# Performance work log

Hardware: AMD Instinct MI355X
Metric: run time of the kernel (lower is better)

## Reference

```python
import jax, jax.numpy as jnp
import numpy as np

B, T, D, H = 4, 4096, 1024, 64

def setup_inputs() -> dict:
    key = jax.random.key(0)
    k1, k2, k3, k4 = jax.random.split(key, 4)
    x = jax.random.normal(k1, (B, T, D), dtype=jnp.float32)
    Wk = jax.random.normal(k2, (D, H), dtype=jnp.float32) * (D ** -0.5)
    Wq = jax.random.normal(k3, (D, H), dtype=jnp.float32) * (D ** -0.5)
    Wv = jax.random.normal(k4, (D, H), dtype=jnp.float32) * (D ** -0.5)
    return {"x": x, "Wk": Wk, "Wq": Wq, "Wv": Wv}

def reference(x, Wk, Wq, Wv):
    # single-head causal self-attention (dropout inactive: training=False)
    k = x @ Wk  # [B,T,H]
    q = x @ Wq  # [B,T,H]
    v = x @ Wv  # [B,T,H]
    scale = jnp.float32(1.0) / jnp.sqrt(jnp.float32(H))
    wei = jnp.einsum('bth,bsh->bts', q, k) * scale  # [B,T,T]
    t = x.shape[1]
    causal = jnp.tril(jnp.ones((t, t), dtype=bool))[None, :, :]
    wei = jnp.where(causal, wei, jnp.float32(-jnp.inf))
    wei = jax.nn.softmax(wei, axis=-1)
    out = jnp.einsum('bts,bsh->bth', wei, v)  # [B,T,H]
    return out
```

## Files before the change

### kernel.cpp

```cpp
#include <hip/hip_runtime.h>

typedef __bf16 bf16_t;
typedef __bf16 bf16x8 __attribute__((ext_vector_type(8)));
typedef __bf16 bf16x4 __attribute__((ext_vector_type(4)));
typedef float  f32x4  __attribute__((ext_vector_type(4)));
typedef float  f32x16 __attribute__((ext_vector_type(16)));

#define B_  4
#define T_  4096
#define H_  64
#define BT  (B_*T_)

#define QSCALE 0.1803368801111204f

#define NSLOT_PB 576
#define NSLOT    2304

#define WS_KFR  0x000000u
#define WS_QFR  0x200000u
#define WS_VFR  0x400000u
#define WS_WT   0x600000u
#define WS_POUT 0x680000u
#define WS_PL   0xF80000u

#define MFMA16(a,b,c) __builtin_amdgcn_mfma_f32_16x16x32_bf16((a),(b),(c),0,0,0)
#define MFMA32(a,b,c) __builtin_amdgcn_mfma_f32_32x32x16_bf16((a),(b),(c),0,0,0)

__device__ __forceinline__ unsigned pk2(float a, float b) {
  union { __bf16 h[2]; unsigned u; } u_;
  u_.h[0] = (__bf16)a; u_.h[1] = (__bf16)b;
  return u_.u;
}

__device__ __forceinline__ f32x16 zero16() {
  f32x16 z;
#pragma unroll
  for (int i = 0; i < 16; ++i) z[i] = 0.f;
  return z;
}

__global__ __launch_bounds__(256) void wtrans_kernel(
    const float* __restrict__ Wk, const float* __restrict__ Wq,
    const float* __restrict__ Wv, bf16_t* __restrict__ WT) {
  __shared__ float lw[64][65];
  int w  = blockIdx.x >> 4;
  int kc = blockIdx.x & 15;
  const float* W = (w == 0) ? Wk : (w == 1) ? Wq : Wv;
  float sc = (w == 1) ? QSCALE : 1.0f;
  int t = threadIdx.x;
  int rr = t >> 2, c0 = (t & 3) * 16;
  const float* src = W + (size_t)(kc*64 + rr)*64 + c0;
#pragma unroll
  for (int j = 0; j < 4; ++j) {
    float4 v = *reinterpret_cast<const float4*>(src + j*4);
    lw[rr][c0+j*4+0] = v.x; lw[rr][c0+j*4+1] = v.y;
    lw[rr][c0+j*4+2] = v.z; lw[rr][c0+j*4+3] = v.w;
  }
  __syncthreads();
  int nl = t >> 2, kl0 = (t & 3) * 16;
  bf16_t* dst = WT + (size_t)(w*64 + nl)*1024 + kc*64 + kl0;
  bf16x8 o0, o1;
#pragma unroll
  for (int j = 0; j < 8; ++j) o0[j] = (bf16_t)(lw[kl0+j][nl] * sc);
#pragma unroll
  for (int j = 0; j < 8; ++j) o1[j] = (bf16_t)(lw[kl0+8+j][nl] * sc);
  *reinterpret_cast<bf16x8*>(dst)     = o0;
  *reinterpret_cast<bf16x8*>(dst + 8) = o1;
}

__global__ __launch_bounds__(256) void proj_kernel(
    const float* __restrict__ x, const bf16_t* __restrict__ WT,
    bf16_t* __restrict__ kfr, bf16_t* __restrict__ qfr, bf16_t* __restrict__ vfr) {
  __shared__ __bf16 xs[2][32][72];
  int tid  = threadIdx.x;
  int wv   = tid >> 6;
  int lane = tid & 63;
  int col  = lane & 15;
  int g    = lane >> 4;
  int m0   = blockIdx.x * 32;
  int nbase = wv * 48;

  f32x4 zero4 = {0.f, 0.f, 0.f, 0.f};
  f32x4 acc[2][3];
#pragma unroll
  for (int i = 0; i < 2; ++i)
#pragma unroll
    for (int j = 0; j < 3; ++j) acc[i][j] = zero4;

  int srow = tid >> 3;
  int scol = (tid & 7) * 8;
  const float* xrow = x + (size_t)(m0 + srow)*1024 + scol;

  float4 a0 = *reinterpret_cast<const float4*>(xrow);
  float4 a1 = *reinterpret_cast<const float4*>(xrow + 4);
  float4 b0 = *reinterpret_cast<const float4*>(xrow + 64);
  float4 b1 = *reinterpret_cast<const float4*>(xrow + 68);
  {
    bf16x8 pk = { (bf16_t)a0.x,(bf16_t)a0.y,(bf16_t)a0.z,(bf16_t)a0.w,
                  (bf16_t)a1.x,(bf16_t)a1.y,(bf16_t)a1.z,(bf16_t)a1.w };
    *reinterpret_cast<bf16x8*>(&xs[0][srow][scol]) = pk;
  }

  for (int t = 0; t < 16; ++t) {
    int kc = t * 64;
    int cur = t & 1;
    __syncthreads();
    if (t + 2 < 16) {
      const float* p = xrow + (t+2)*64;
      if ((t & 1) == 0) { a0 = *reinterpret_cast<const float4*>(p);
                          a1 = *reinterpret_cast<const float4*>(p + 4); }
      else              { b0 = *reinterpret_cast<const float4*>(p);
                          b1 = *reinterpret_cast<const float4*>(p + 4); }
    }
#pragma unroll
    for (int kk = 0; kk < 2; ++kk) {
      int ko = kk*32 + g*8;
      bf16x8 f0 = *(const bf16x8*)&xs[cur][ 0 + col][ko];
      bf16x8 f1 = *(const bf16x8*)&xs[cur][16 + col][ko];
#pragma unroll
      for (int nti = 0; nti < 3; ++nti) {
        const bf16_t* wp = WT + (size_t)(nbase + nti*16 + col)*1024 + kc + ko;
        bf16x8 bfr = *(const bf16x8*)wp;
        acc[0][nti] = MFMA16(f0, bfr, acc[0][nti]);
        acc[1][nti] = MFMA16(f1, bfr, acc[1][nti]);
      }
    }
    if (t + 1 < 16) {
      bf16x8 pk;
      if ((t & 1) == 0)
        pk = bf16x8{ (bf16_t)b0.x,(bf16_t)b0.y,(bf16_t)b0.z,(bf16_t)b0.w,
                     (bf16_t)b1.x,(bf16_t)b1.y,(bf16_t)b1.z,(bf16_t)b1.w };
      else
        pk = bf16x8{ (bf16_t)a0.x,(bf16_t)a0.y,(bf16_t)a0.z,(bf16_t)a0.w,
                     (bf16_t)a1.x,(bf16_t)a1.y,(bf16_t)a1.z,(bf16_t)a1.w };
      *reinterpret_cast<bf16x8*>(&xs[cur^1][srow][scol]) = pk;
    }
  }
#pragma unroll
  for (int mt = 0; mt < 2; ++mt) {
    int row0 = m0 + mt*16 + 4*g;
#pragma unroll
    for (int nti = 0; nti < 3; ++nti) {
      int n = nbase + nti*16 + col;
      f32x4 v = acc[mt][nti];
      if (n < 128) {
        int h = n & 63;
        bf16_t* base = (n < 64) ? kfr : qfr;
#pragma unroll
        for (int r = 0; r < 4; ++r) {
          int t2 = row0 + r;
          size_t idx = (size_t)((t2>>6)*8 + ((t2>>5)&1)*4 + (h>>4))*512
                     + (size_t)((t2&31) + ((h>>3)&1)*32)*8 + (h&7);
          base[idx] = (bf16_t)v[r];
        }
      } else {
        int h = n - 128;
        size_t idx = (size_t)((row0>>6)*8 + ((h>>5)&1)*4 + ((row0>>4)&3))*512
                   + (size_t)((h&31) + ((row0>>3)&1)*32)*8 + (row0&7);
        bf16x4 pk = { (bf16_t)v[0], (bf16_t)v[1], (bf16_t)v[2], (bf16_t)v[3] };
        *reinterpret_cast<bf16x4*>(&vfr[idx]) = pk;
      }
    }
  }
}

__global__ __launch_bounds__(64) void attn_kernel(
    const bf16_t* __restrict__ qfr, const bf16_t* __restrict__ kfr,
    const bf16_t* __restrict__ vfr, bf16_t* __restrict__ pout,
    float* __restrict__ pl) {
  int l  = threadIdx.x;
  int ql = l & 31;
  int hi = l >> 5;

  int bidx = blockIdx.x;
  int b = bidx / NSLOT_PB;
  int s = bidx - b * NSLOT_PB;
  s = NSLOT_PB - 1 - s;
  int a = 0;
#pragma unroll
  for (int aa = 1; aa < 8; ++aa) if (8*aa*(aa+1) <= s) a = aa;
  int r2 = s - 8*a*(a+1);
  int qd = r2 / (a+1);
  int c  = r2 - qd*(a+1);
  int jt = 16*a + qd;
  int slot = b*NSLOT_PB + s;

  int q0    = jt << 5;
  int kv_lo = c << 9;
  int kv_hi = min(kv_lo + 512, q0 + 32);
  int ntiles = (kv_hi - kv_lo + 63) >> 6;
  int qg = q0 + ql;

  const bf16_t* qb = qfr + (size_t)((b*T_ + q0) >> 6)*4096
                   + (size_t)((q0 >> 5) & 1)*2048 + l*8;
  bf16x8 qf0 = *(const bf16x8*)(qb);
  bf16x8 qf1 = *(const bf16x8*)(qb + 512);
  bf16x8 qf2 = *(const bf16x8*)(qb + 1024);
  bf16x8 qf3 = *(const bf16x8*)(qb + 1536);

  const bf16_t* kfb = kfr + (size_t)(b*T_)*64 + l*8;
  const bf16_t* vfb = vfr + (size_t)(b*T_)*64 + l*8;

  bf16x8 kA0,kA1,kA2,kA3, kB0,kB1,kB2,kB3;
#define LOADK(kvt_) do { const bf16_t* kp_ = kfb + (size_t)(kvt_)*64;          \
    kA0=*(const bf16x8*)(kp_);        kA1=*(const bf16x8*)(kp_+512);           \
    kA2=*(const bf16x8*)(kp_+1024);   kA3=*(const bf16x8*)(kp_+1536);          \
    kB0=*(const bf16x8*)(kp_+2048);   kB1=*(const bf16x8*)(kp_+2560);          \
    kB2=*(const bf16x8*)(kp_+3072);   kB3=*(const bf16x8*)(kp_+3584); } while(0)

  LOADK(kv_lo);

  f32x16 oA = zero16(), oB = zero16();
  float l_ = 0.f;

  for (int t = 0; t < ntiles; ++t) {
    int kvt = kv_lo + t*64;
    const bf16_t* vp = vfb + (size_t)kvt*64;
    bf16x8 vA0 = *(const bf16x8*)(vp);
    bf16x8 vA1 = *(const bf16x8*)(vp + 512);
    bf16x8 vA2 = *(const bf16x8*)(vp + 1024);
    bf16x8 vA3 = *(const bf16x8*)(vp + 1536);
    bf16x8 vB0 = *(const bf16x8*)(vp + 2048);
    bf16x8 vB1 = *(const bf16x8*)(vp + 2560);
    bf16x8 vB2 = *(const bf16x8*)(vp + 3072);
    bf16x8 vB3 = *(const bf16x8*)(vp + 3584);

    f32x16 sA = zero16(), sB = zero16();
    sA = MFMA32(kA0, qf0, sA); sB = MFMA32(kB0, qf0, sB);
    sA = MFMA32(kA1, qf1, sA); sB = MFMA32(kB1, qf1, sB);
    sA = MFMA32(kA2, qf2, sA); sB = MFMA32(kB2, qf2, sB);
    sA = MFMA32(kA3, qf3, sA); sB = MFMA32(kB3, qf3, sB);

    if (t + 1 < ntiles) LOADK(kvt + 64);

    if (kvt + 63 > q0) {
#pragma unroll
      for (int r = 0; r < 16; ++r) {
        int kvo = kvt + (r&3) + 8*(r>>2) + 4*hi;
        if (kvo > qg)      sA[r] = -1e30f;
        if (kvo + 32 > qg) sB[r] = -1e30f;
      }
    }

    float pA[16], pB[16];
    float ts = 0.f;
#pragma unroll
    for (int r = 0; r < 16; ++r) { pA[r] = exp2f(sA[r]); ts += pA[r]; }
#pragma unroll
    for (int r = 0; r < 16; ++r) { pB[r] = exp2f(sB[r]); ts += pB[r]; }
    l_ += ts + __shfl_xor(ts, 32);

    bf16x8 p0, p1, p2, p3;
#define MKSLICES(P, F0, F1) do {                                               \
    unsigned w0 = pk2(P[0],P[1]),   w1 = pk2(P[2],P[3]);                       \
    unsigned w2 = pk2(P[4],P[5]),   w3 = pk2(P[6],P[7]);                       \
    unsigned w4 = pk2(P[8],P[9]),   w5 = pk2(P[10],P[11]);                     \
    unsigned w6 = pk2(P[12],P[13]), w7 = pk2(P[14],P[15]);                     \
    unsigned x0 = (unsigned)__shfl_xor((int)w0,32);                            \
    unsigned x1 = (unsigned)__shfl_xor((int)w1,32);                            \
    unsigned x2 = (unsigned)__shfl_xor((int)w2,32);                            \
    unsigned x3 = (unsigned)__shfl_xor((int)w3,32);                            \
    unsigned x4 = (unsigned)__shfl_xor((int)w4,32);                            \
    unsigned x5 = (unsigned)__shfl_xor((int)w5,32);                            \
    unsigned x6 = (unsigned)__shfl_xor((int)w6,32);                            \
    unsigned x7 = (unsigned)__shfl_xor((int)w7,32);                            \
    union { unsigned d[4]; bf16x8 v; } u0_, u1_;                               \
    u0_.d[0] = hi ? x2 : w0;  u0_.d[1] = hi ? x3 : w1;                         \
    u0_.d[2] = hi ? w2 : x0;  u0_.d[3] = hi ? w3 : x1;                         \
    u1_.d[0] = hi ? x6 : w4;  u1_.d[1] = hi ? x7 : w5;                         \
    u1_.d[2] = hi ? w6 : x4;  u1_.d[3] = hi ? w7 : x5;                         \
    F0 = u0_.v; F1 = u1_.v; } while(0)
    MKSLICES(pA, p0, p1);
    MKSLICES(pB, p2, p3);

    oA = MFMA32(vA0, p0, oA); oB = MFMA32(vB0, p0, oB);
    oA = MFMA32(vA1, p1, oA); oB = MFMA32(vB1, p1, oB);
    oA = MFMA32(vA2, p2, oA); oB = MFMA32(vB2, p2, oB);
    oA = MFMA32(vA3, p3, oA); oB = MFMA32(vB3, p3, oB);
  }

  bf16_t* po = pout + (size_t)slot * 2048;
#pragma unroll
  for (int r = 0; r < 16; ++r) {
    int h = (r&3) + 8*(r>>2) + 4*hi;
    po[h*32 + ql]      = (bf16_t)oA[r];
    po[(h+32)*32 + ql] = (bf16_t)oB[r];
  }
  if (l < 32) pl[(size_t)slot*32 + l] = l_;
}

__global__ __launch_bounds__(256) void combine_kernel(
    const bf16_t* __restrict__ pout, const float* __restrict__ pl,
    float* __restrict__ out) {
  int blk = blockIdx.x;
  int b  = blk >> 7;
  int jt = blk & 127;
  int tid = threadIdx.x;
  int wv = tid >> 6;
  int l  = tid & 63;
  int a  = jt >> 4;
  int nch = a + 1;
  int slot0 = b*NSLOT_PB + 8*a*(a+1) + (jt & 15)*(a+1);

  float oacc[8], lacc[8];
#pragma unroll
  for (int q = 0; q < 8; ++q) { oacc[q] = 0.f; lacc[q] = 0.f; }
  for (int c2 = 0; c2 < nch; ++c2) {
    const bf16_t* pp = pout + (size_t)(slot0 + c2)*2048 + l*32 + wv*8;
    bf16x8 o8 = *(const bf16x8*)pp;
    const float* plc = pl + (size_t)(slot0 + c2)*32 + wv*8;
#pragma unroll
    for (int q = 0; q < 8; ++q) { oacc[q] += (float)o8[q]; lacc[q] += plc[q]; }
  }
  float* op = out + ((size_t)b*T_ + (size_t)jt*32 + wv*8)*64 + l;
#pragma unroll
  for (int q = 0; q < 8; ++q) op[(size_t)q*64] = oacc[q] / lacc[q];
}

extern "C" void kernel_launch(void* const* d_in, const int* in_sizes, int n_in,
                              void* d_out, int out_size, void* d_ws, size_t ws_size,
                              hipStream_t stream) {
  (void)in_sizes; (void)n_in; (void)out_size; (void)ws_size;
  const float* x  = (const float*)d_in[0];
  const float* Wk = (const float*)d_in[1];
  const float* Wq = (const float*)d_in[2];
  const float* Wv = (const float*)d_in[3];
  char* ws = (char*)d_ws;
  bf16_t* kfr  = (bf16_t*)(ws + WS_KFR);
  bf16_t* qfr  = (bf16_t*)(ws + WS_QFR);
  bf16_t* vfr  = (bf16_t*)(ws + WS_VFR);
  bf16_t* WT   = (bf16_t*)(ws + WS_WT);
  bf16_t* pout = (bf16_t*)(ws + WS_POUT);
  float*  pl   = (float*)(ws + WS_PL);
  float*  outp = (float*)d_out;

  hipLaunchKernelGGL(wtrans_kernel,  dim3(48),    dim3(256), 0, stream, Wk, Wq, Wv, WT);
  hipLaunchKernelGGL(proj_kernel,    dim3(512),   dim3(256), 0, stream, x, WT, kfr, qfr, vfr);
  hipLaunchKernelGGL(attn_kernel,    dim3(NSLOT), dim3(64),  0, stream, qfr, kfr, vfr, pout, pl);
  hipLaunchKernelGGL(combine_kernel, dim3(512),   dim3(256), 0, stream, pout, pl, outp);
}
```

Before: 70.71 us.

## Halve KV split chunk, widen projection blocks, and raise MFMA wave priority

```diff
diff --git a/kernel.cpp b/kernel.cpp
--- a/kernel.cpp
+++ b/kernel.cpp
@@ -13,15 +13,15 @@
 
 #define QSCALE 0.1803368801111204f
 
-#define NSLOT_PB 576
-#define NSLOT    2304
-
-#define WS_KFR  0x000000u
-#define WS_QFR  0x200000u
-#define WS_VFR  0x400000u
-#define WS_WT   0x600000u
-#define WS_POUT 0x680000u
-#define WS_PL   0xF80000u
+#define NSLOT_PB 1088
+#define NSLOT    4352
+
+#define WS_KFR  0x0000000u
+#define WS_QFR  0x0200000u
+#define WS_VFR  0x0400000u
+#define WS_WT   0x0600000u
+#define WS_POUT 0x0680000u
+#define WS_PL   0x1780000u
 
 #define MFMA16(a,b,c) __builtin_amdgcn_mfma_f32_16x16x32_bf16((a),(b),(c),0,0,0)
 #define MFMA32(a,b,c) __builtin_amdgcn_mfma_f32_32x32x16_bf16((a),(b),(c),0,0,0)
@@ -68,98 +68,81 @@
   *reinterpret_cast<bf16x8*>(dst + 8) = o1;
 }
 
-__global__ __launch_bounds__(256) void proj_kernel(
+__global__ __launch_bounds__(512) void proj_kernel(
     const float* __restrict__ x, const bf16_t* __restrict__ WT,
     bf16_t* __restrict__ kfr, bf16_t* __restrict__ qfr, bf16_t* __restrict__ vfr) {
   __shared__ __bf16 xs[2][32][72];
   int tid  = threadIdx.x;
   int wv   = tid >> 6;
+  int wm   = wv >> 2;
+  int wn   = wv & 3;
   int lane = tid & 63;
   int col  = lane & 15;
   int g    = lane >> 4;
   int m0   = blockIdx.x * 32;
-  int nbase = wv * 48;
+  int nbase = wn * 48;
 
   f32x4 zero4 = {0.f, 0.f, 0.f, 0.f};
-  f32x4 acc[2][3];
-#pragma unroll
-  for (int i = 0; i < 2; ++i)
-#pragma unroll
-    for (int j = 0; j < 3; ++j) acc[i][j] = zero4;
-
-  int srow = tid >> 3;
-  int scol = (tid & 7) * 8;
+  f32x4 acc[3] = {zero4, zero4, zero4};
+
+  int srow = tid >> 4;
+  int scol = (tid & 15) * 4;
   const float* xrow = x + (size_t)(m0 + srow)*1024 + scol;
 
   float4 a0 = *reinterpret_cast<const float4*>(xrow);
-  float4 a1 = *reinterpret_cast<const float4*>(xrow + 4);
   float4 b0 = *reinterpret_cast<const float4*>(xrow + 64);
-  float4 b1 = *reinterpret_cast<const float4*>(xrow + 68);
   {
-    bf16x8 pk = { (bf16_t)a0.x,(bf16_t)a0.y,(bf16_t)a0.z,(bf16_t)a0.w,
-                  (bf16_t)a1.x,(bf16_t)a1.y,(bf16_t)a1.z,(bf16_t)a1.w };
-    *reinterpret_cast<bf16x8*>(&xs[0][srow][scol]) = pk;
+    bf16x4 pk = { (bf16_t)a0.x,(bf16_t)a0.y,(bf16_t)a0.z,(bf16_t)a0.w };
+    *reinterpret_cast<bf16x4*>(&xs[0][srow][scol]) = pk;
   }
 
   for (int t = 0; t < 16; ++t) {
+    __syncthreads();
     int kc = t * 64;
     int cur = t & 1;
-    __syncthreads();
     if (t + 2 < 16) {
       const float* p = xrow + (t+2)*64;
-      if ((t & 1) == 0) { a0 = *reinterpret_cast<const float4*>(p);
-                          a1 = *reinterpret_cast<const float4*>(p + 4); }
-      else              { b0 = *reinterpret_cast<const float4*>(p);
-                          b1 = *reinterpret_cast<const float4*>(p + 4); }
+      if ((t & 1) == 0) a0 = *reinterpret_cast<const float4*>(p);
+      else              b0 = *reinterpret_cast<const float4*>(p);
     }
 #pragma unroll
     for (int kk = 0; kk < 2; ++kk) {
       int ko = kk*32 + g*8;
-      bf16x8 f0 = *(const bf16x8*)&xs[cur][ 0 + col][ko];
-      bf16x8 f1 = *(const bf16x8*)&xs[cur][16 + col][ko];
+      bf16x8 f0 = *(const bf16x8*)&xs[cur][wm*16 + col][ko];
 #pragma unroll
       for (int nti = 0; nti < 3; ++nti) {
         const bf16_t* wp = WT + (size_t)(nbase + nti*16 + col)*1024 + kc + ko;
         bf16x8 bfr = *(const bf16x8*)wp;
-        acc[0][nti] = MFMA16(f0, bfr, acc[0][nti]);
-        acc[1][nti] = MFMA16(f1, bfr, acc[1][nti]);
+        acc[nti] = MFMA16(f0, bfr, acc[nti]);
       }
     }
     if (t + 1 < 16) {
-      bf16x8 pk;
-      if ((t & 1) == 0)
-        pk = bf16x8{ (bf16_t)b0.x,(bf16_t)b0.y,(bf16_t)b0.z,(bf16_t)b0.w,
-                     (bf16_t)b1.x,(bf16_t)b1.y,(bf16_t)b1.z,(bf16_t)b1.w };
-      else
-        pk = bf16x8{ (bf16_t)a0.x,(bf16_t)a0.y,(bf16_t)a0.z,(bf16_t)a0.w,
-                     (bf16_t)a1.x,(bf16_t)a1.y,(bf16_t)a1.z,(bf16_t)a1.w };
-      *reinterpret_cast<bf16x8*>(&xs[cur^1][srow][scol]) = pk;
-    }
-  }
-#pragma unroll
-  for (int mt = 0; mt < 2; ++mt) {
-    int row0 = m0 + mt*16 + 4*g;
-#pragma unroll
-    for (int nti = 0; nti < 3; ++nti) {
-      int n = nbase + nti*16 + col;
-      f32x4 v = acc[mt][nti];
-      if (n < 128) {
-        int h = n & 63;
-        bf16_t* base = (n < 64) ? kfr : qfr;
-#pragma unroll
-        for (int r = 0; r < 4; ++r) {
-          int t2 = row0 + r;
-          size_t idx = (size_t)((t2>>6)*8 + ((t2>>5)&1)*4 + (h>>4))*512
-                     + (size_t)((t2&31) + ((h>>3)&1)*32)*8 + (h&7);
-          base[idx] = (bf16_t)v[r];
-        }
-      } else {
-        int h = n - 128;
-        size_t idx = (size_t)((row0>>6)*8 + ((h>>5)&1)*4 + ((row0>>4)&3))*512
-                   + (size_t)((h&31) + ((row0>>3)&1)*32)*8 + (row0&7);
-        bf16x4 pk = { (bf16_t)v[0], (bf16_t)v[1], (bf16_t)v[2], (bf16_t)v[3] };
-        *reinterpret_cast<bf16x4*>(&vfr[idx]) = pk;
+      float4 sv = ((t & 1) == 0) ? b0 : a0;
+      bf16x4 pk = { (bf16_t)sv.x,(bf16_t)sv.y,(bf16_t)sv.z,(bf16_t)sv.w };
+      *reinterpret_cast<bf16x4*>(&xs[cur^1][srow][scol]) = pk;
+    }
+  }
+  int row0 = m0 + wm*16 + 4*g;
+#pragma unroll
+  for (int nti = 0; nti < 3; ++nti) {
+    int n = nbase + nti*16 + col;
+    f32x4 v = acc[nti];
+    if (n < 128) {
+      int h = n & 63;
+      bf16_t* base = (n < 64) ? kfr : qfr;
+#pragma unroll
+      for (int r = 0; r < 4; ++r) {
+        int t2 = row0 + r;
+        size_t idx = (size_t)((t2>>6)*8 + ((t2>>5)&1)*4 + (h>>4))*512
+                   + (size_t)((t2&31) + ((h>>3)&1)*32)*8 + (h&7);
+        base[idx] = (bf16_t)v[r];
       }
+    } else {
+      int h = n - 128;
+      size_t idx = (size_t)((row0>>6)*8 + ((h>>5)&1)*4 + ((row0>>4)&3))*512
+                 + (size_t)((h&31) + ((row0>>3)&1)*32)*8 + (row0&7);
+      bf16x4 pk = { (bf16_t)v[0], (bf16_t)v[1], (bf16_t)v[2], (bf16_t)v[3] };
+      *reinterpret_cast<bf16x4*>(&vfr[idx]) = pk;
     }
   }
 }
@@ -178,16 +161,16 @@
   s = NSLOT_PB - 1 - s;
   int a = 0;
 #pragma unroll
-  for (int aa = 1; aa < 8; ++aa) if (8*aa*(aa+1) <= s) a = aa;
-  int r2 = s - 8*a*(a+1);
+  for (int aa = 1; aa < 16; ++aa) if (4*aa*(aa+1) <= s) a = aa;
+  int r2 = s - 4*a*(a+1);
   int qd = r2 / (a+1);
   int c  = r2 - qd*(a+1);
-  int jt = 16*a + qd;
+  int jt = 8*a + qd;
   int slot = b*NSLOT_PB + s;
 
   int q0    = jt << 5;
-  int kv_lo = c << 9;
-  int kv_hi = min(kv_lo + 512, q0 + 32);
+  int kv_lo = c << 8;
+  int kv_hi = min(kv_lo + 256, q0 + 32);
   int ntiles = (kv_hi - kv_lo + 63) >> 6;
   int qg = q0 + ql;
 
@@ -226,10 +209,12 @@
     bf16x8 vB3 = *(const bf16x8*)(vp + 3584);
 
     f32x16 sA = zero16(), sB = zero16();
+    __builtin_amdgcn_s_setprio(1);
     sA = MFMA32(kA0, qf0, sA); sB = MFMA32(kB0, qf0, sB);
     sA = MFMA32(kA1, qf1, sA); sB = MFMA32(kB1, qf1, sB);
     sA = MFMA32(kA2, qf2, sA); sB = MFMA32(kB2, qf2, sB);
     sA = MFMA32(kA3, qf3, sA); sB = MFMA32(kB3, qf3, sB);
+    __builtin_amdgcn_s_setprio(0);
 
     if (t + 1 < ntiles) LOADK(kvt + 64);
 
@@ -273,10 +258,12 @@
     MKSLICES(pA, p0, p1);
     MKSLICES(pB, p2, p3);
 
+    __builtin_amdgcn_s_setprio(1);
     oA = MFMA32(vA0, p0, oA); oB = MFMA32(vB0, p0, oB);
     oA = MFMA32(vA1, p1, oA); oB = MFMA32(vB1, p1, oB);
     oA = MFMA32(vA2, p2, oA); oB = MFMA32(vB2, p2, oB);
     oA = MFMA32(vA3, p3, oA); oB = MFMA32(vB3, p3, oB);
+    __builtin_amdgcn_s_setprio(0);
   }
 
   bf16_t* po = pout + (size_t)slot * 2048;
@@ -298,9 +285,9 @@
   int tid = threadIdx.x;
   int wv = tid >> 6;
   int l  = tid & 63;
-  int a  = jt >> 4;
+  int a  = jt >> 3;
   int nch = a + 1;
-  int slot0 = b*NSLOT_PB + 8*a*(a+1) + (jt & 15)*(a+1);
+  int slot0 = b*NSLOT_PB + 4*a*(a+1) + (jt & 7)*(a+1);
 
   float oacc[8], lacc[8];
 #pragma unroll
@@ -335,7 +322,7 @@
   float*  outp = (float*)d_out;
 
   hipLaunchKernelGGL(wtrans_kernel,  dim3(48),    dim3(256), 0, stream, Wk, Wq, Wv, WT);
-  hipLaunchKernelGGL(proj_kernel,    dim3(512),   dim3(256), 0, stream, x, WT, kfr, qfr, vfr);
+  hipLaunchKernelGGL(proj_kernel,    dim3(512),   dim3(512), 0, stream, x, WT, kfr, qfr, vfr);
   hipLaunchKernelGGL(attn_kernel,    dim3(NSLOT), dim3(64),  0, stream, qfr, kfr, vfr, pout, pl);
   hipLaunchKernelGGL(combine_kernel, dim3(512),   dim3(256), 0, stream, pout, pl, outp);
 }
```

Measured after the change: 89.67 us. +26.8%, slower.
